# Kernel optimization log

Hardware: AMD Instinct MI355X
Metric: run time of the kernel (lower is better)

## Reference

```python
import jax, jax.numpy as jnp
import numpy as np

N, E, NFEAT, NHID = 50000, 800000, 256, 128
EPS = 1e-5


def setup_inputs() -> dict:
    key = jax.random.key(0)
    ks = jax.random.split(key, 12)
    s = 0.05
    return {
        "x": jax.random.normal(ks[0], (N, NFEAT), jnp.float32),
        "adj": jax.random.randint(ks[1], (2, E), 0, N, jnp.int32),
        "features": jax.random.uniform(ks[2], (E,), jnp.float32),
        "W_in": jax.random.normal(ks[3], (NHID, NFEAT), jnp.float32) * s,
        "b_in": jnp.zeros((NHID,), jnp.float32),
        "W1_rel": jax.random.normal(ks[4], (NHID, NHID), jnp.float32) * s,
        "b1_rel": jnp.zeros((NHID,), jnp.float32),
        "W1_root": jax.random.normal(ks[5], (NHID, NHID), jnp.float32) * s,
        "W2_rel": jax.random.normal(ks[6], (NHID, NHID), jnp.float32) * s,
        "b2_rel": jnp.zeros((NHID,), jnp.float32),
        "W2_root": jax.random.normal(ks[7], (NHID, NHID), jnp.float32) * s,
        "gamma": jnp.ones((NHID,), jnp.float32),
        "beta": jnp.zeros((NHID,), jnp.float32),
    }


def _graph_conv(h, src, dst, ew, W_rel, b_rel, W_root):
    # torch_geometric GraphConv (aggr='add'):
    #   out_i = W_rel @ (sum_{j->i} e_ji * h_j) + b_rel + W_root @ h_i
    msg = h[src] * ew[:, None]                       # [E, NHID] gather
    agg = jax.ops.segment_sum(msg, dst, num_segments=N)  # [N, NHID] scatter-add
    return agg @ W_rel.T + b_rel + h @ W_root.T


def _batch_norm(h, gamma, beta):
    mu = h.mean(axis=0)
    var = h.var(axis=0)
    return (h - mu) * jax.lax.rsqrt(var + EPS) * gamma + beta


def reference(x, adj, features, W_in, b_in, W1_rel, b1_rel, W1_root,
              W2_rel, b2_rel, W2_root, gamma, beta):
    src, dst = adj[0], adj[1]
    h = jax.nn.relu(x @ W_in.T + b_in)               # linear_in + relu (dropout=identity in eval)
    h = _graph_conv(h, src, dst, features, W1_rel, b1_rel, W1_root)
    h = jax.nn.relu(_batch_norm(h, gamma, beta))     # batch1 + relu
    h = _graph_conv(h, src, dst, features, W2_rel, b2_rel, W2_root)
    return _batch_norm(h, gamma, beta)               # batch1 reused (per source)
```

## Files before the change

### kernel.cpp

```cpp
#include <hip/hip_runtime.h>
#include <hip/hip_bf16.h>

#define NNODES 50000
#define NEDGES 800000
#define NF 256
#define NH 128
#define BN_EPS 1e-5f
#define MTILES (NNODES / 16)
#define GEMM_BLOCKS 512
#define CONV_BLOCKS2 512
#define NBUCKETS 196
#define BCAP 4608
#define SCAT_BLOCKS ((NEDGES + 2047) / 2048)
#define WCONV_BLOCKS (98304 / 256)

typedef __attribute__((ext_vector_type(8))) __bf16 bf16x8;
typedef __attribute__((ext_vector_type(4))) float floatx4;

__device__ __forceinline__ __hip_bfloat16 f2bf(float f) { return __float2bfloat16(f); }
__device__ __forceinline__ float bits2f(unsigned short b) {
    union { unsigned u; float f; } u; u.u = ((unsigned)b) << 16; return u.f;
}

__device__ __forceinline__ bf16x8 cvt8(const float* __restrict__ p) {
    floatx4 a0 = *(const floatx4*)p;
    floatx4 a1 = *(const floatx4*)(p + 4);
    bf16x8 r;
    r[0] = (__bf16)a0[0]; r[1] = (__bf16)a0[1]; r[2] = (__bf16)a0[2]; r[3] = (__bf16)a0[3];
    r[4] = (__bf16)a1[0]; r[5] = (__bf16)a1[1]; r[6] = (__bf16)a1[2]; r[7] = (__bf16)a1[3];
    return r;
}

__global__ __launch_bounds__(256) void prep_kernel(
    const int* __restrict__ adj, const float* __restrict__ ew,
    int* __restrict__ gcursor, uint2* __restrict__ pairbuf,
    unsigned char* __restrict__ nodebuf,
    const float* __restrict__ W_in, const float* __restrict__ W1r,
    const float* __restrict__ W1o, const float* __restrict__ W2r,
    const float* __restrict__ W2o, __hip_bfloat16* __restrict__ wbf)
{
    __shared__ int cnt[NBUCKETS];
    __shared__ int base[NBUCKETS];
    const int tid = threadIdx.x;

    if (blockIdx.x >= SCAT_BLOCKS) {
        const int i = (blockIdx.x - SCAT_BLOCKS) * 256 + tid;
        const float* src; int off;
        if (i < 32768)      { src = W_in; off = i; }
        else if (i < 49152) { src = W1r;  off = i - 32768; }
        else if (i < 65536) { src = W1o;  off = i - 49152; }
        else if (i < 81920) { src = W2r;  off = i - 65536; }
        else                { src = W2o;  off = i - 81920; }
        wbf[i] = f2bf(src[off]);
        return;
    }

    if (tid < NBUCKETS) cnt[tid] = 0;
    __syncthreads();
    const int e0 = blockIdx.x * 2048;
    #pragma unroll
    for (int i = 0; i < 8; ++i) {
        const int e = e0 + i * 256 + tid;
        if (e < NEDGES) atomicAdd(&cnt[adj[NEDGES + e] >> 8], 1);
    }
    __syncthreads();
    if (tid < NBUCKETS) {
        base[tid] = tid * BCAP + atomicAdd(&gcursor[tid], cnt[tid]);
        cnt[tid] = 0;
    }
    __syncthreads();
    #pragma unroll
    for (int i = 0; i < 8; ++i) {
        const int e = e0 + i * 256 + tid;
        if (e >= NEDGES) continue;
        const int dst = adj[NEDGES + e];
        const int b = dst >> 8;
        const int off = atomicAdd(&cnt[b], 1);
        const int slot = base[b] + off;
        if (slot < (b + 1) * BCAP) {
            pairbuf[slot] = make_uint2((unsigned)adj[e], __float_as_uint(ew[e]));
            nodebuf[slot] = (unsigned char)(dst & 255);
        }
    }
}

__global__ __launch_bounds__(256) void bucket_sort_kernel(
    const int* __restrict__ gcursor, const uint2* __restrict__ pairbuf,
    const unsigned char* __restrict__ nodebuf, uint2* __restrict__ sorted,
    int* __restrict__ rowptr, int* __restrict__ rowend)
{
    const int b = blockIdx.x;
    const int tid = threadIdx.x;
    const int capbase = b * BCAP;
    int n = gcursor[b];
    if (n > BCAP) n = BCAP;

    __shared__ int cnt[256];
    __shared__ int s[256];
    cnt[tid] = 0;
    __syncthreads();
    for (int j = tid; j < n; j += 256)
        atomicAdd(&cnt[nodebuf[capbase + j]], 1);
    __syncthreads();
    const int v = cnt[tid];
    s[tid] = v;
    __syncthreads();
    for (int off = 1; off < 256; off <<= 1) {
        const int t = (tid >= off) ? s[tid - off] : 0;
        __syncthreads();
        s[tid] += t;
        __syncthreads();
    }
    const int excl = s[tid] - v;
    const int node = b * 256 + tid;
    if (node < NNODES) {
        rowptr[node] = capbase + excl;
        rowend[node] = capbase + excl + v;
    }
    cnt[tid] = excl;
    __syncthreads();
    for (int j = tid; j < n; j += 256) {
        const int nd = nodebuf[capbase + j];
        const int pos = atomicAdd(&cnt[nd], 1);
        sorted[capbase + pos] = pairbuf[capbase + j];
    }
}

__global__ __launch_bounds__(256, 2) void gemm_in_kernel(
    const float* __restrict__ X, const __hip_bfloat16* __restrict__ W,
    const float* __restrict__ bias, __hip_bfloat16* __restrict__ out)
{
    const int waveG = blockIdx.x * 4 + (threadIdx.x >> 6);
    const int lane = threadIdx.x & 63;
    const int half = waveG & 1;
    const int ar = lane & 15;
    const int q  = lane >> 4;

    bf16x8 bw[4][8];
    float bv[4];
    #pragma unroll
    for (int t = 0; t < 4; ++t) {
        const int row = half * 64 + t * 16 + ar;
        bv[t] = bias[row];
        #pragma unroll
        for (int k = 0; k < 8; ++k)
            bw[t][k] = *(const bf16x8*)(W + (size_t)row * NF + k * 32 + q * 8);
    }

    for (int strip = waveG >> 1; strip < MTILES; strip += GEMM_BLOCKS * 2) {
        const int m0 = strip << 4;
        floatx4 acc[4] = {};
        #pragma unroll
        for (int k = 0; k < 8; ++k) {
            const bf16x8 a = cvt8(X + (size_t)(m0 + ar) * NF + k * 32 + q * 8);
            #pragma unroll
            for (int t = 0; t < 4; ++t)
                acc[t] = __builtin_amdgcn_mfma_f32_16x16x32_bf16(a, bw[t][k], acc[t], 0, 0, 0);
        }
        #pragma unroll
        for (int t = 0; t < 4; ++t) {
            const int col = half * 64 + t * 16 + ar;
            #pragma unroll
            for (int r = 0; r < 4; ++r) {
                const float v = fmaxf(acc[t][r] + bv[t], 0.f);
                out[(size_t)(m0 + q * 4 + r) * NH + col] = f2bf(v);
            }
        }
    }
}

__global__ __launch_bounds__(256) void gather_kernel(
    const uint2* __restrict__ sorted, const int* __restrict__ rowptr,
    const int* __restrict__ rowend,
    const __hip_bfloat16* __restrict__ h, __hip_bfloat16* __restrict__ agg)
{
    const int node = blockIdx.x * 4 + (threadIdx.x >> 6);
    if (node >= NNODES) return;
    const int lane = threadIdx.x & 63;
    const int beg = rowptr[node];
    const int end = rowend[node];
    const unsigned short* hb = (const unsigned short*)h;

    float a0[8] = {}, a1[8] = {};

    int j = beg;
    if ((j & 1) && j < end) {
        const uint2 ev = sorted[j++];
        const float w = __uint_as_float(ev.y);
        const unsigned raw = *(const unsigned*)(hb + (size_t)ev.x * NH + lane * 2);
        a0[0] += w * bits2f((unsigned short)(raw & 0xffffu));
        a1[0] += w * bits2f((unsigned short)(raw >> 16));
    }
    for (; j + 8 <= end; j += 8) {
        const uint4 e01 = *(const uint4*)(sorted + j);
        const uint4 e23 = *(const uint4*)(sorted + j + 2);
        const uint4 e45 = *(const uint4*)(sorted + j + 4);
        const uint4 e67 = *(const uint4*)(sorted + j + 6);
        const unsigned r0 = *(const unsigned*)(hb + (size_t)e01.x * NH + lane * 2);
        const unsigned r1 = *(const unsigned*)(hb + (size_t)e01.z * NH + lane * 2);
        const unsigned r2 = *(const unsigned*)(hb + (size_t)e23.x * NH + lane * 2);
        const unsigned r3 = *(const unsigned*)(hb + (size_t)e23.z * NH + lane * 2);
        const unsigned r4 = *(const unsigned*)(hb + (size_t)e45.x * NH + lane * 2);
        const unsigned r5 = *(const unsigned*)(hb + (size_t)e45.z * NH + lane * 2);
        const unsigned r6 = *(const unsigned*)(hb + (size_t)e67.x * NH + lane * 2);
        const unsigned r7 = *(const unsigned*)(hb + (size_t)e67.z * NH + lane * 2);
        const float w0 = __uint_as_float(e01.y), w1 = __uint_as_float(e01.w);
        const float w2 = __uint_as_float(e23.y), w3 = __uint_as_float(e23.w);
        const float w4 = __uint_as_float(e45.y), w5 = __uint_as_float(e45.w);
        const float w6 = __uint_as_float(e67.y), w7 = __uint_as_float(e67.w);
        a0[0] += w0 * bits2f((unsigned short)(r0 & 0xffffu));
        a1[0] += w0 * bits2f((unsigned short)(r0 >> 16));
        a0[1] += w1 * bits2f((unsigned short)(r1 & 0xffffu));
        a1[1] += w1 * bits2f((unsigned short)(r1 >> 16));
        a0[2] += w2 * bits2f((unsigned short)(r2 & 0xffffu));
        a1[2] += w2 * bits2f((unsigned short)(r2 >> 16));
        a0[3] += w3 * bits2f((unsigned short)(r3 & 0xffffu));
        a1[3] += w3 * bits2f((unsigned short)(r3 >> 16));
        a0[4] += w4 * bits2f((unsigned short)(r4 & 0xffffu));
        a1[4] += w4 * bits2f((unsigned short)(r4 >> 16));
        a0[5] += w5 * bits2f((unsigned short)(r5 & 0xffffu));
        a1[5] += w5 * bits2f((unsigned short)(r5 >> 16));
        a0[6] += w6 * bits2f((unsigned short)(r6 & 0xffffu));
        a1[6] += w6 * bits2f((unsigned short)(r6 >> 16));
        a0[7] += w7 * bits2f((unsigned short)(r7 & 0xffffu));
        a1[7] += w7 * bits2f((unsigned short)(r7 >> 16));
    }
    for (; j + 2 <= end; j += 2) {
        const uint4 e01 = *(const uint4*)(sorted + j);
        const unsigned r0 = *(const unsigned*)(hb + (size_t)e01.x * NH + lane * 2);
        const unsigned r1 = *(const unsigned*)(hb + (size_t)e01.z * NH + lane * 2);
        const float w0 = __uint_as_float(e01.y), w1 = __uint_as_float(e01.w);
        a0[0] += w0 * bits2f((unsigned short)(r0 & 0xffffu));
        a1[0] += w0 * bits2f((unsigned short)(r0 >> 16));
        a0[1] += w1 * bits2f((unsigned short)(r1 & 0xffffu));
        a1[1] += w1 * bits2f((unsigned short)(r1 >> 16));
    }
    if (j < end) {
        const uint2 ev = sorted[j];
        const float w = __uint_as_float(ev.y);
        const unsigned raw = *(const unsigned*)(hb + (size_t)ev.x * NH + lane * 2);
        a0[0] += w * bits2f((unsigned short)(raw & 0xffffu));
        a1[0] += w * bits2f((unsigned short)(raw >> 16));
    }
    const float f0 = ((a0[0] + a0[1]) + (a0[2] + a0[3])) + ((a0[4] + a0[5]) + (a0[6] + a0[7]));
    const float f1 = ((a1[0] + a1[1]) + (a1[2] + a1[3])) + ((a1[4] + a1[5]) + (a1[6] + a1[7]));
    unsigned o = ((unsigned)__bfloat16_as_ushort(f2bf(f1)) << 16) |
                 (unsigned)__bfloat16_as_ushort(f2bf(f0));
    *(unsigned*)((unsigned short*)agg + (size_t)node * NH + lane * 2) = o;
}

#define LROW 528

__global__ __launch_bounds__(512, 4) void gemm_conv_kernel(
    const __hip_bfloat16* __restrict__ agg, const __hip_bfloat16* __restrict__ h,
    const __hip_bfloat16* __restrict__ Wrel, const __hip_bfloat16* __restrict__ Wroot,
    const float* __restrict__ bias, float* __restrict__ out,
    float* __restrict__ stats)
{
    __shared__ char wlds[128 * LROW];
    __shared__ float sst[256];
    const int tid = threadIdx.x;
    if (tid < 256) sst[tid] = 0.f;

    {
        const int r = tid >> 2, part = tid & 3;
        const __hip_bfloat16* src = (part < 2 ? Wrel : Wroot) + (size_t)r * NH + (part & 1) * 64;
        char* dst = wlds + r * LROW + part * 128;
        #pragma unroll
        for (int j = 0; j < 8; ++j)
            *(bf16x8*)(dst + j * 16) = *(const bf16x8*)(src + j * 8);
    }
    __syncthreads();

    const int lane = tid & 63;
    const int ar = lane & 15;
    const int q  = lane >> 4;
    const int strip = blockIdx.x * 8 + (tid >> 6);

    if (strip < MTILES) {
        const int m0 = strip << 4;
        float bv[8];
        #pragma unroll
        for (int t = 0; t < 8; ++t) bv[t] = bias[t * 16 + ar];

        floatx4 acc[8] = {};
        const char* wl = wlds + ar * LROW + q * 16;
        #pragma unroll
        for (int kk = 0; kk < 4; ++kk) {
            const bf16x8 a = *(const bf16x8*)(agg + (size_t)(m0 + ar) * NH + kk * 32 + q * 8);
            #pragma unroll
            for (int t = 0; t < 8; ++t)
                acc[t] = __builtin_amdgcn_mfma_f32_16x16x32_bf16(
                    a, *(const bf16x8*)(wl + t * (16 * LROW) + kk * 64), acc[t], 0, 0, 0);
        }
        #pragma unroll
        for (int kk = 0; kk < 4; ++kk) {
            const bf16x8 a = *(const bf16x8*)(h + (size_t)(m0 + ar) * NH + kk * 32 + q * 8);
            #pragma unroll
            for (int t = 0; t < 8; ++t)
                acc[t] = __builtin_amdgcn_mfma_f32_16x16x32_bf16(
                    a, *(const bf16x8*)(wl + t * (16 * LROW) + 256 + kk * 64), acc[t], 0, 0, 0);
        }

        #pragma unroll
        for (int t = 0; t < 8; ++t) {
            float s1 = 0.f, s2 = 0.f;
            #pragma unroll
            for (int r = 0; r < 4; ++r) {
                const float v = acc[t][r] + bv[t];
                out[(size_t)(m0 + q * 4 + r) * NH + t * 16 + ar] = v;
                s1 += v; s2 += v * v;
            }
            s1 += __shfl_xor(s1, 16, 64); s1 += __shfl_xor(s1, 32, 64);
            s2 += __shfl_xor(s2, 16, 64); s2 += __shfl_xor(s2, 32, 64);
            if (q == 0) {
                atomicAdd(&sst[t * 16 + ar], s1);
                atomicAdd(&sst[128 + t * 16 + ar], s2);
            }
        }
    }
    __syncthreads();
    if (tid < 256) unsafeAtomicAdd(&stats[tid], sst[tid]);
}

__global__ __launch_bounds__(256) void bn_relu_bf16_kernel(
    const float* __restrict__ t, const float* __restrict__ stats,
    const float* __restrict__ gamma, const float* __restrict__ beta,
    __hip_bfloat16* __restrict__ out)
{
    const size_t i = (size_t)blockIdx.x * blockDim.x + threadIdx.x;
    const int c = (int)(i & (NH - 1));
    const float inv_n = 1.0f / (float)NNODES;
    const float mu = stats[c] * inv_n;
    const float var = stats[128 + c] * inv_n - mu * mu;
    const float rs = rsqrtf(var + BN_EPS);
    float v = (t[i] - mu) * rs * gamma[c] + beta[c];
    out[i] = f2bf(fmaxf(v, 0.f));
}

__global__ __launch_bounds__(256) void bn_f32_kernel(
    const float* __restrict__ t, const float* __restrict__ stats,
    const float* __restrict__ gamma, const float* __restrict__ beta,
    float* __restrict__ out)
{
    const size_t i = (size_t)blockIdx.x * blockDim.x + threadIdx.x;
    const int c = (int)(i & (NH - 1));
    const float inv_n = 1.0f / (float)NNODES;
    const float mu = stats[c] * inv_n;
    const float var = stats[128 + c] * inv_n - mu * mu;
    const float rs = rsqrtf(var + BN_EPS);
    out[i] = (t[i] - mu) * rs * gamma[c] + beta[c];
}


extern "C" void kernel_launch(void* const* d_in, const int* in_sizes, int n_in,
                              void* d_out, int out_size, void* d_ws, size_t ws_size,
                              hipStream_t stream)
{
    const float* x    = (const float*)d_in[0];
    const int*   adj  = (const int*)d_in[1];
    const float* ew   = (const float*)d_in[2];
    const float* W_in = (const float*)d_in[3];
    const float* b_in = (const float*)d_in[4];
    const float* W1r  = (const float*)d_in[5];
    const float* b1   = (const float*)d_in[6];
    const float* W1o  = (const float*)d_in[7];
    const float* W2r  = (const float*)d_in[8];
    const float* b2   = (const float*)d_in[9];
    const float* W2o  = (const float*)d_in[10];
    const float* gmm  = (const float*)d_in[11];
    const float* bta  = (const float*)d_in[12];
    float* out = (float*)d_out;
    float* t   = (float*)d_out;

    char* ws = (char*)d_ws;
    __hip_bfloat16* h0  = (__hip_bfloat16*)ws; ws += (size_t)NNODES * NH * 2;
    __hip_bfloat16* h1  = (__hip_bfloat16*)ws; ws += (size_t)NNODES * NH * 2;
    __hip_bfloat16* agg = (__hip_bfloat16*)ws; ws += (size_t)NNODES * NH * 2;
    uint2*          sorted  = (uint2*)ws;      ws += (size_t)NBUCKETS * BCAP * 8;
    uint2*          pairbuf = (uint2*)ws;      ws += (size_t)NBUCKETS * BCAP * 8;
    unsigned char*  nodebuf = (unsigned char*)ws; ws += (size_t)NBUCKETS * BCAP;
    int*            rowptr  = (int*)ws;        ws += NNODES * 4;
    int*            rowend  = (int*)ws;        ws += NNODES * 4;
    int*            gcursor = (int*)ws;        ws += 256 * 4;
    float*          st1     = (float*)ws;      ws += 256 * 4;
    float*          st2     = (float*)ws;      ws += 256 * 4;
    __hip_bfloat16* wbf     = (__hip_bfloat16*)ws; ws += 98304 * 2;

    const __hip_bfloat16* Wb_in = wbf;
    const __hip_bfloat16* Wb1r  = wbf + 32768;
    const __hip_bfloat16* Wb1o  = wbf + 49152;
    const __hip_bfloat16* Wb2r  = wbf + 65536;
    const __hip_bfloat16* Wb2o  = wbf + 81920;

    const int node_blocks = (NNODES + 3) / 4;
    const int bn_blocks   = (NNODES * NH) / 256;

    hipMemsetAsync(gcursor, 0, 3 * 256 * 4, stream);
    prep_kernel<<<SCAT_BLOCKS + WCONV_BLOCKS, 256, 0, stream>>>(
        adj, ew, gcursor, pairbuf, nodebuf, W_in, W1r, W1o, W2r, W2o, wbf);
    bucket_sort_kernel<<<NBUCKETS, 256, 0, stream>>>(gcursor, pairbuf, nodebuf,
                                                     sorted, rowptr, rowend);

    gemm_in_kernel<<<GEMM_BLOCKS, 256, 0, stream>>>(x, Wb_in, b_in, h0);
    gather_kernel<<<node_blocks, 256, 0, stream>>>(sorted, rowptr, rowend, h0, agg);
    gemm_conv_kernel<<<CONV_BLOCKS2, 512, 0, stream>>>(agg, h0, Wb1r, Wb1o, b1, t, st1);
    bn_relu_bf16_kernel<<<bn_blocks, 256, 0, stream>>>(t, st1, gmm, bta, h1);

    gather_kernel<<<node_blocks, 256, 0, stream>>>(sorted, rowptr, rowend, h1, agg);
    gemm_conv_kernel<<<CONV_BLOCKS2, 512, 0, stream>>>(agg, h1, Wb2r, Wb2o, b2, t, st2);
    bn_f32_kernel<<<bn_blocks, 256, 0, stream>>>(t, st2, gmm, bta, out);
}
```

Before: 304.9 us.

## Fuse edge gather into graph-conv GEMM via per-wave LDS tile; vectorize BN kernels

Merges the gather kernel and the conv GEMM into one kernel. Each wave aggregates 16 nodes sequentially into an LDS tile, then runs MFMA with weights read directly from global memory instead of staging them in LDS. This removes the agg buffer round trip and one launch per layer. The risk is that gather latency is now serialized per wave, with less parallelism per node and no weight reuse through LDS. The BN kernels are also changed to process four elements per thread with vector loads and stores.

```diff
diff --git a/kernel.cpp b/kernel.cpp
--- a/kernel.cpp
+++ b/kernel.cpp
@@ -8,11 +8,12 @@
 #define BN_EPS 1e-5f
 #define MTILES (NNODES / 16)
 #define GEMM_BLOCKS 512
-#define CONV_BLOCKS2 512
+#define FUSE_BLOCKS ((MTILES + 3) / 4)
 #define NBUCKETS 196
 #define BCAP 4608
 #define SCAT_BLOCKS ((NEDGES + 2047) / 2048)
 #define WCONV_BLOCKS (98304 / 256)
+#define APITCH 272
 
 typedef __attribute__((ext_vector_type(8))) __bf16 bf16x8;
 typedef __attribute__((ext_vector_type(4))) float floatx4;
@@ -169,129 +170,111 @@
     }
 }
 
-__global__ __launch_bounds__(256) void gather_kernel(
+__global__ __launch_bounds__(256, 4) void gather_conv_kernel(
     const uint2* __restrict__ sorted, const int* __restrict__ rowptr,
-    const int* __restrict__ rowend,
-    const __hip_bfloat16* __restrict__ h, __hip_bfloat16* __restrict__ agg)
-{
-    const int node = blockIdx.x * 4 + (threadIdx.x >> 6);
-    if (node >= NNODES) return;
-    const int lane = threadIdx.x & 63;
-    const int beg = rowptr[node];
-    const int end = rowend[node];
-    const unsigned short* hb = (const unsigned short*)h;
-
-    float a0[8] = {}, a1[8] = {};
-
-    int j = beg;
-    if ((j & 1) && j < end) {
-        const uint2 ev = sorted[j++];
-        const float w = __uint_as_float(ev.y);
-        const unsigned raw = *(const unsigned*)(hb + (size_t)ev.x * NH + lane * 2);
-        a0[0] += w * bits2f((unsigned short)(raw & 0xffffu));
-        a1[0] += w * bits2f((unsigned short)(raw >> 16));
-    }
-    for (; j + 8 <= end; j += 8) {
-        const uint4 e01 = *(const uint4*)(sorted + j);
-        const uint4 e23 = *(const uint4*)(sorted + j + 2);
-        const uint4 e45 = *(const uint4*)(sorted + j + 4);
-        const uint4 e67 = *(const uint4*)(sorted + j + 6);
-        const unsigned r0 = *(const unsigned*)(hb + (size_t)e01.x * NH + lane * 2);
-        const unsigned r1 = *(const unsigned*)(hb + (size_t)e01.z * NH + lane * 2);
-        const unsigned r2 = *(const unsigned*)(hb + (size_t)e23.x * NH + lane * 2);
-        const unsigned r3 = *(const unsigned*)(hb + (size_t)e23.z * NH + lane * 2);
-        const unsigned r4 = *(const unsigned*)(hb + (size_t)e45.x * NH + lane * 2);
-        const unsigned r5 = *(const unsigned*)(hb + (size_t)e45.z * NH + lane * 2);
-        const unsigned r6 = *(const unsigned*)(hb + (size_t)e67.x * NH + lane * 2);
-        const unsigned r7 = *(const unsigned*)(hb + (size_t)e67.z * NH + lane * 2);
-        const float w0 = __uint_as_float(e01.y), w1 = __uint_as_float(e01.w);
-        const float w2 = __uint_as_float(e23.y), w3 = __uint_as_float(e23.w);
-        const float w4 = __uint_as_float(e45.y), w5 = __uint_as_float(e45.w);
-        const float w6 = __uint_as_float(e67.y), w7 = __uint_as_float(e67.w);
-        a0[0] += w0 * bits2f((unsigned short)(r0 & 0xffffu));
-        a1[0] += w0 * bits2f((unsigned short)(r0 >> 16));
-        a0[1] += w1 * bits2f((unsigned short)(r1 & 0xffffu));
-        a1[1] += w1 * bits2f((unsigned short)(r1 >> 16));
-        a0[2] += w2 * bits2f((unsigned short)(r2 & 0xffffu));
-        a1[2] += w2 * bits2f((unsigned short)(r2 >> 16));
-        a0[3] += w3 * bits2f((unsigned short)(r3 & 0xffffu));
-        a1[3] += w3 * bits2f((unsigned short)(r3 >> 16));
-        a0[4] += w4 * bits2f((unsigned short)(r4 & 0xffffu));
-        a1[4] += w4 * bits2f((unsigned short)(r4 >> 16));
-        a0[5] += w5 * bits2f((unsigned short)(r5 & 0xffffu));
-        a1[5] += w5 * bits2f((unsigned short)(r5 >> 16));
-        a0[6] += w6 * bits2f((unsigned short)(r6 & 0xffffu));
-        a1[6] += w6 * bits2f((unsigned short)(r6 >> 16));
-        a0[7] += w7 * bits2f((unsigned short)(r7 & 0xffffu));
-        a1[7] += w7 * bits2f((unsigned short)(r7 >> 16));
-    }
-    for (; j + 2 <= end; j += 2) {
-        const uint4 e01 = *(const uint4*)(sorted + j);
-        const unsigned r0 = *(const unsigned*)(hb + (size_t)e01.x * NH + lane * 2);
-        const unsigned r1 = *(const unsigned*)(hb + (size_t)e01.z * NH + lane * 2);
-        const float w0 = __uint_as_float(e01.y), w1 = __uint_as_float(e01.w);
-        a0[0] += w0 * bits2f((unsigned short)(r0 & 0xffffu));
-        a1[0] += w0 * bits2f((unsigned short)(r0 >> 16));
-        a0[1] += w1 * bits2f((unsigned short)(r1 & 0xffffu));
-        a1[1] += w1 * bits2f((unsigned short)(r1 >> 16));
-    }
-    if (j < end) {
-        const uint2 ev = sorted[j];
-        const float w = __uint_as_float(ev.y);
-        const unsigned raw = *(const unsigned*)(hb + (size_t)ev.x * NH + lane * 2);
-        a0[0] += w * bits2f((unsigned short)(raw & 0xffffu));
-        a1[0] += w * bits2f((unsigned short)(raw >> 16));
-    }
-    const float f0 = ((a0[0] + a0[1]) + (a0[2] + a0[3])) + ((a0[4] + a0[5]) + (a0[6] + a0[7]));
-    const float f1 = ((a1[0] + a1[1]) + (a1[2] + a1[3])) + ((a1[4] + a1[5]) + (a1[6] + a1[7]));
-    unsigned o = ((unsigned)__bfloat16_as_ushort(f2bf(f1)) << 16) |
-                 (unsigned)__bfloat16_as_ushort(f2bf(f0));
-    *(unsigned*)((unsigned short*)agg + (size_t)node * NH + lane * 2) = o;
-}
-
-#define LROW 528
-
-__global__ __launch_bounds__(512, 4) void gemm_conv_kernel(
-    const __hip_bfloat16* __restrict__ agg, const __hip_bfloat16* __restrict__ h,
+    const int* __restrict__ rowend, const __hip_bfloat16* __restrict__ h,
     const __hip_bfloat16* __restrict__ Wrel, const __hip_bfloat16* __restrict__ Wroot,
     const float* __restrict__ bias, float* __restrict__ out,
     float* __restrict__ stats)
 {
-    __shared__ char wlds[128 * LROW];
+    __shared__ char alds[4 * 16 * APITCH];
     __shared__ float sst[256];
     const int tid = threadIdx.x;
-    if (tid < 256) sst[tid] = 0.f;
-
-    {
-        const int r = tid >> 2, part = tid & 3;
-        const __hip_bfloat16* src = (part < 2 ? Wrel : Wroot) + (size_t)r * NH + (part & 1) * 64;
-        char* dst = wlds + r * LROW + part * 128;
-        #pragma unroll
-        for (int j = 0; j < 8; ++j)
-            *(bf16x8*)(dst + j * 16) = *(const bf16x8*)(src + j * 8);
-    }
-    __syncthreads();
-
+    sst[tid] = 0.f;
+    __syncthreads();
+
+    const int w = tid >> 6;
     const int lane = tid & 63;
-    const int ar = lane & 15;
-    const int q  = lane >> 4;
-    const int strip = blockIdx.x * 8 + (tid >> 6);
+    const int strip = blockIdx.x * 4 + w;
+    const unsigned short* hb = (const unsigned short*)h;
+    char* atile = alds + w * (16 * APITCH);
 
     if (strip < MTILES) {
         const int m0 = strip << 4;
-        float bv[8];
-        #pragma unroll
-        for (int t = 0; t < 8; ++t) bv[t] = bias[t * 16 + ar];
-
+
+        for (int i = 0; i < 16; ++i) {
+            const int node = m0 + i;
+            const int beg = rowptr[node];
+            const int end = rowend[node];
+
+            float a0[8] = {}, a1[8] = {};
+            int j = beg;
+            if ((j & 1) && j < end) {
+                const uint2 ev = sorted[j++];
+                const float wt = __uint_as_float(ev.y);
+                const unsigned raw = *(const unsigned*)(hb + (size_t)ev.x * NH + lane * 2);
+                a0[0] += wt * bits2f((unsigned short)(raw & 0xffffu));
+                a1[0] += wt * bits2f((unsigned short)(raw >> 16));
+            }
+            for (; j + 8 <= end; j += 8) {
+                const uint4 e01 = *(const uint4*)(sorted + j);
+                const uint4 e23 = *(const uint4*)(sorted + j + 2);
+                const uint4 e45 = *(const uint4*)(sorted + j + 4);
+                const uint4 e67 = *(const uint4*)(sorted + j + 6);
+                const unsigned r0 = *(const unsigned*)(hb + (size_t)e01.x * NH + lane * 2);
+                const unsigned r1 = *(const unsigned*)(hb + (size_t)e01.z * NH + lane * 2);
+                const unsigned r2 = *(const unsigned*)(hb + (size_t)e23.x * NH + lane * 2);
+                const unsigned r3 = *(const unsigned*)(hb + (size_t)e23.z * NH + lane * 2);
+                const unsigned r4 = *(const unsigned*)(hb + (size_t)e45.x * NH + lane * 2);
+                const unsigned r5 = *(const unsigned*)(hb + (size_t)e45.z * NH + lane * 2);
+                const unsigned r6 = *(const unsigned*)(hb + (size_t)e67.x * NH + lane * 2);
+                const unsigned r7 = *(const unsigned*)(hb + (size_t)e67.z * NH + lane * 2);
+                const float w0 = __uint_as_float(e01.y), w1 = __uint_as_float(e01.w);
+                const float w2 = __uint_as_float(e23.y), w3 = __uint_as_float(e23.w);
+                const float w4 = __uint_as_float(e45.y), w5 = __uint_as_float(e45.w);
+                const float w6 = __uint_as_float(e67.y), w7 = __uint_as_float(e67.w);
+                a0[0] += w0 * bits2f((unsigned short)(r0 & 0xffffu));
+                a1[0] += w0 * bits2f((unsigned short)(r0 >> 16));
+                a0[1] += w1 * bits2f((unsigned short)(r1 & 0xffffu));
+                a1[1] += w1 * bits2f((unsigned short)(r1 >> 16));
+                a0[2] += w2 * bits2f((unsigned short)(r2 & 0xffffu));
+                a1[2] += w2 * bits2f((unsigned short)(r2 >> 16));
+                a0[3] += w3 * bits2f((unsigned short)(r3 & 0xffffu));
+                a1[3] += w3 * bits2f((unsigned short)(r3 >> 16));
+                a0[4] += w4 * bits2f((unsigned short)(r4 & 0xffffu));
+                a1[4] += w4 * bits2f((unsigned short)(r4 >> 16));
+                a0[5] += w5 * bits2f((unsigned short)(r5 & 0xffffu));
+                a1[5] += w5 * bits2f((unsigned short)(r5 >> 16));
+                a0[6] += w6 * bits2f((unsigned short)(r6 & 0xffffu));
+                a1[6] += w6 * bits2f((unsigned short)(r6 >> 16));
+                a0[7] += w7 * bits2f((unsigned short)(r7 & 0xffffu));
+                a1[7] += w7 * bits2f((unsigned short)(r7 >> 16));
+            }
+            for (; j + 2 <= end; j += 2) {
+                const uint4 e01 = *(const uint4*)(sorted + j);
+                const unsigned r0 = *(const unsigned*)(hb + (size_t)e01.x * NH + lane * 2);
+                const unsigned r1 = *(const unsigned*)(hb + (size_t)e01.z * NH + lane * 2);
+                const float w0 = __uint_as_float(e01.y), w1 = __uint_as_float(e01.w);
+                a0[0] += w0 * bits2f((unsigned short)(r0 & 0xffffu));
+                a1[0] += w0 * bits2f((unsigned short)(r0 >> 16));
+                a0[1] += w1 * bits2f((unsigned short)(r1 & 0xffffu));
+                a1[1] += w1 * bits2f((unsigned short)(r1 >> 16));
+            }
+            if (j < end) {
+                const uint2 ev = sorted[j];
+                const float wt = __uint_as_float(ev.y);
+                const unsigned raw = *(const unsigned*)(hb + (size_t)ev.x * NH + lane * 2);
+                a0[0] += wt * bits2f((unsigned short)(raw & 0xffffu));
+                a1[0] += wt * bits2f((unsigned short)(raw >> 16));
+            }
+            const float f0 = ((a0[0] + a0[1]) + (a0[2] + a0[3])) + ((a0[4] + a0[5]) + (a0[6] + a0[7]));
+            const float f1 = ((a1[0] + a1[1]) + (a1[2] + a1[3])) + ((a1[4] + a1[5]) + (a1[6] + a1[7]));
+            const unsigned o = ((unsigned)__bfloat16_as_ushort(f2bf(f1)) << 16) |
+                               (unsigned)__bfloat16_as_ushort(f2bf(f0));
+            *(unsigned*)(atile + i * APITCH + lane * 4) = o;
+        }
+
+        const int ar = lane & 15;
+        const int q  = lane >> 4;
         floatx4 acc[8] = {};
-        const char* wl = wlds + ar * LROW + q * 16;
         #pragma unroll
         for (int kk = 0; kk < 4; ++kk) {
-            const bf16x8 a = *(const bf16x8*)(agg + (size_t)(m0 + ar) * NH + kk * 32 + q * 8);
+            const bf16x8 a = *(const bf16x8*)(atile + ar * APITCH + kk * 64 + q * 16);
             #pragma unroll
             for (int t = 0; t < 8; ++t)
                 acc[t] = __builtin_amdgcn_mfma_f32_16x16x32_bf16(
-                    a, *(const bf16x8*)(wl + t * (16 * LROW) + kk * 64), acc[t], 0, 0, 0);
+                    a, *(const bf16x8*)(Wrel + (size_t)(t * 16 + ar) * NH + kk * 32 + q * 8),
+                    acc[t], 0, 0, 0);
         }
         #pragma unroll
         for (int kk = 0; kk < 4; ++kk) {
@@ -299,15 +282,17 @@
             #pragma unroll
             for (int t = 0; t < 8; ++t)
                 acc[t] = __builtin_amdgcn_mfma_f32_16x16x32_bf16(
-                    a, *(const bf16x8*)(wl + t * (16 * LROW) + 256 + kk * 64), acc[t], 0, 0, 0);
+                    a, *(const bf16x8*)(Wroot + (size_t)(t * 16 + ar) * NH + kk * 32 + q * 8),
+                    acc[t], 0, 0, 0);
         }
 
         #pragma unroll
         for (int t = 0; t < 8; ++t) {
+            const float bvt = bias[t * 16 + ar];
             float s1 = 0.f, s2 = 0.f;
             #pragma unroll
             for (int r = 0; r < 4; ++r) {
-                const float v = acc[t][r] + bv[t];
+                const float v = acc[t][r] + bvt;
                 out[(size_t)(m0 + q * 4 + r) * NH + t * 16 + ar] = v;
                 s1 += v; s2 += v * v;
             }
@@ -320,7 +305,7 @@
         }
     }
     __syncthreads();
-    if (tid < 256) unsafeAtomicAdd(&stats[tid], sst[tid]);
+    unsafeAtomicAdd(&stats[tid], sst[tid]);
 }
 
 __global__ __launch_bounds__(256) void bn_relu_bf16_kernel(
@@ -328,14 +313,21 @@
     const float* __restrict__ gamma, const float* __restrict__ beta,
     __hip_bfloat16* __restrict__ out)
 {
-    const size_t i = (size_t)blockIdx.x * blockDim.x + threadIdx.x;
-    const int c = (int)(i & (NH - 1));
+    const size_t i = ((size_t)blockIdx.x * 256 + threadIdx.x) * 4;
     const float inv_n = 1.0f / (float)NNODES;
-    const float mu = stats[c] * inv_n;
-    const float var = stats[128 + c] * inv_n - mu * mu;
-    const float rs = rsqrtf(var + BN_EPS);
-    float v = (t[i] - mu) * rs * gamma[c] + beta[c];
-    out[i] = f2bf(fmaxf(v, 0.f));
+    const floatx4 v = *(const floatx4*)(t + i);
+    ushort4 o;
+    unsigned short* op = (unsigned short*)&o;
+    #pragma unroll
+    for (int j = 0; j < 4; ++j) {
+        const int c = (int)((i + j) & (NH - 1));
+        const float mu = stats[c] * inv_n;
+        const float var = stats[128 + c] * inv_n - mu * mu;
+        const float rs = rsqrtf(var + BN_EPS);
+        const float y = (v[j] - mu) * rs * gamma[c] + beta[c];
+        op[j] = __bfloat16_as_ushort(f2bf(fmaxf(y, 0.f)));
+    }
+    *(ushort4*)((unsigned short*)out + i) = o;
 }
 
 __global__ __launch_bounds__(256) void bn_f32_kernel(
@@ -343,13 +335,19 @@
     const float* __restrict__ gamma, const float* __restrict__ beta,
     float* __restrict__ out)
 {
-    const size_t i = (size_t)blockIdx.x * blockDim.x + threadIdx.x;
-    const int c = (int)(i & (NH - 1));
+    const size_t i = ((size_t)blockIdx.x * 256 + threadIdx.x) * 4;
     const float inv_n = 1.0f / (float)NNODES;
-    const float mu = stats[c] * inv_n;
-    const float var = stats[128 + c] * inv_n - mu * mu;
-    const float rs = rsqrtf(var + BN_EPS);
-    out[i] = (t[i] - mu) * rs * gamma[c] + beta[c];
+    const floatx4 v = *(const floatx4*)(t + i);
+    floatx4 o;
+    #pragma unroll
+    for (int j = 0; j < 4; ++j) {
+        const int c = (int)((i + j) & (NH - 1));
+        const float mu = stats[c] * inv_n;
+        const float var = stats[128 + c] * inv_n - mu * mu;
+        const float rs = rsqrtf(var + BN_EPS);
+        o[j] = (v[j] - mu) * rs * gamma[c] + beta[c];
+    }
+    *(floatx4*)(out + i) = o;
 }
 
 
@@ -376,7 +374,6 @@
     char* ws = (char*)d_ws;
     __hip_bfloat16* h0  = (__hip_bfloat16*)ws; ws += (size_t)NNODES * NH * 2;
     __hip_bfloat16* h1  = (__hip_bfloat16*)ws; ws += (size_t)NNODES * NH * 2;
-    __hip_bfloat16* agg = (__hip_bfloat16*)ws; ws += (size_t)NNODES * NH * 2;
     uint2*          sorted  = (uint2*)ws;      ws += (size_t)NBUCKETS * BCAP * 8;
     uint2*          pairbuf = (uint2*)ws;      ws += (size_t)NBUCKETS * BCAP * 8;
     unsigned char*  nodebuf = (unsigned char*)ws; ws += (size_t)NBUCKETS * BCAP;
@@ -393,8 +390,7 @@
     const __hip_bfloat16* Wb2r  = wbf + 65536;
     const __hip_bfloat16* Wb2o  = wbf + 81920;
 
-    const int node_blocks = (NNODES + 3) / 4;
-    const int bn_blocks   = (NNODES * NH) / 256;
+    const int bn_blocks = (NNODES * NH) / (256 * 4);
 
     hipMemsetAsync(gcursor, 0, 3 * 256 * 4, stream);
     prep_kernel<<<SCAT_BLOCKS + WCONV_BLOCKS, 256, 0, stream>>>(
@@ -403,11 +399,11 @@
                                                      sorted, rowptr, rowend);
 
     gemm_in_kernel<<<GEMM_BLOCKS, 256, 0, stream>>>(x, Wb_in, b_in, h0);
-    gather_kernel<<<node_blocks, 256, 0, stream>>>(sorted, rowptr, rowend, h0, agg);
-    gemm_conv_kernel<<<CONV_BLOCKS2, 512, 0, stream>>>(agg, h0, Wb1r, Wb1o, b1, t, st1);
+    gather_conv_kernel<<<FUSE_BLOCKS, 256, 0, stream>>>(sorted, rowptr, rowend,
+                                                        h0, Wb1r, Wb1o, b1, t, st1);
     bn_relu_bf16_kernel<<<bn_blocks, 256, 0, stream>>>(t, st1, gmm, bta, h1);
 
-    gather_kernel<<<node_blocks, 256, 0, stream>>>(sorted, rowptr, rowend, h1, agg);
-    gemm_conv_kernel<<<CONV_BLOCKS2, 512, 0, stream>>>(agg, h1, Wb2r, Wb2o, b2, t, st2);
+    gather_conv_kernel<<<FUSE_BLOCKS, 256, 0, stream>>>(sorted, rowptr, rowend,
+                                                        h1, Wb2r, Wb2o, b2, t, st2);
     bn_f32_kernel<<<bn_blocks, 256, 0, stream>>>(t, st2, gmm, bta, out);
 }
```

Measured after the change: 372.3 us. 1.22x slower.

## Fuse batchnorm into conv GEMM via grid barrier; merge input GEMM into prep

Applied to the files above, without the earlier changes.

The input linear GEMM moves into the prep kernel as an extra block range, converting W_in to bf16 on the fly, so it runs concurrently with edge bucketing and the weight conversion and saves a launch. The conv GEMM kernels now keep results in registers, accumulate BN statistics, wait at a spin-wait grid barrier on an atomic counter, then apply batchnorm (plus ReLU for layer 1) and write the output directly. This removes the fp32 intermediate write/read and the two separate BN kernels. The risk is that the barrier deadlocks unless all 512 blocks are co-resident, and the spin adds latency.

```diff
diff --git a/kernel.cpp b/kernel.cpp
--- a/kernel.cpp
+++ b/kernel.cpp
@@ -12,7 +12,9 @@
 #define NBUCKETS 196
 #define BCAP 4608
 #define SCAT_BLOCKS ((NEDGES + 2047) / 2048)
-#define WCONV_BLOCKS (98304 / 256)
+#define WC2_BLOCKS 256
+#define FRONT_BLOCKS (SCAT_BLOCKS + WC2_BLOCKS + GEMM_BLOCKS)
+#define LROW 528
 
 typedef __attribute__((ext_vector_type(8))) __bf16 bf16x8;
 typedef __attribute__((ext_vector_type(4))) float floatx4;
@@ -31,33 +33,76 @@
     return r;
 }
 
-__global__ __launch_bounds__(256) void prep_kernel(
+__global__ __launch_bounds__(256, 2) void front_kernel(
     const int* __restrict__ adj, const float* __restrict__ ew,
     int* __restrict__ gcursor, uint2* __restrict__ pairbuf,
     unsigned char* __restrict__ nodebuf,
-    const float* __restrict__ W_in, const float* __restrict__ W1r,
-    const float* __restrict__ W1o, const float* __restrict__ W2r,
-    const float* __restrict__ W2o, __hip_bfloat16* __restrict__ wbf)
+    const float* __restrict__ W1r, const float* __restrict__ W1o,
+    const float* __restrict__ W2r, const float* __restrict__ W2o,
+    __hip_bfloat16* __restrict__ wbf,
+    const float* __restrict__ X, const float* __restrict__ W_in,
+    const float* __restrict__ b_in, __hip_bfloat16* __restrict__ h0)
 {
     __shared__ int cnt[NBUCKETS];
     __shared__ int base[NBUCKETS];
     const int tid = threadIdx.x;
-
-    if (blockIdx.x >= SCAT_BLOCKS) {
-        const int i = (blockIdx.x - SCAT_BLOCKS) * 256 + tid;
+    const int bid = blockIdx.x;
+
+    if (bid >= SCAT_BLOCKS + WC2_BLOCKS) {
+        const int waveG = (bid - SCAT_BLOCKS - WC2_BLOCKS) * 4 + (tid >> 6);
+        const int lane = tid & 63;
+        const int half = waveG & 1;
+        const int ar = lane & 15;
+        const int q  = lane >> 4;
+
+        bf16x8 bw[4][8];
+        float bv[4];
+        #pragma unroll
+        for (int t = 0; t < 4; ++t) {
+            const int row = half * 64 + t * 16 + ar;
+            bv[t] = b_in[row];
+            #pragma unroll
+            for (int k = 0; k < 8; ++k)
+                bw[t][k] = cvt8(W_in + (size_t)row * NF + k * 32 + q * 8);
+        }
+
+        for (int strip = waveG >> 1; strip < MTILES; strip += GEMM_BLOCKS * 2) {
+            const int m0 = strip << 4;
+            floatx4 acc[4] = {};
+            #pragma unroll
+            for (int k = 0; k < 8; ++k) {
+                const bf16x8 a = cvt8(X + (size_t)(m0 + ar) * NF + k * 32 + q * 8);
+                #pragma unroll
+                for (int t = 0; t < 4; ++t)
+                    acc[t] = __builtin_amdgcn_mfma_f32_16x16x32_bf16(a, bw[t][k], acc[t], 0, 0, 0);
+            }
+            #pragma unroll
+            for (int t = 0; t < 4; ++t) {
+                const int col = half * 64 + t * 16 + ar;
+                #pragma unroll
+                for (int r = 0; r < 4; ++r) {
+                    const float v = fmaxf(acc[t][r] + bv[t], 0.f);
+                    h0[(size_t)(m0 + q * 4 + r) * NH + col] = f2bf(v);
+                }
+            }
+        }
+        return;
+    }
+
+    if (bid >= SCAT_BLOCKS) {
+        const int i = (bid - SCAT_BLOCKS) * 256 + tid;
         const float* src; int off;
-        if (i < 32768)      { src = W_in; off = i; }
-        else if (i < 49152) { src = W1r;  off = i - 32768; }
-        else if (i < 65536) { src = W1o;  off = i - 49152; }
-        else if (i < 81920) { src = W2r;  off = i - 65536; }
-        else                { src = W2o;  off = i - 81920; }
+        if (i < 16384)      { src = W1r; off = i; }
+        else if (i < 32768) { src = W1o; off = i - 16384; }
+        else if (i < 49152) { src = W2r; off = i - 32768; }
+        else                { src = W2o; off = i - 49152; }
         wbf[i] = f2bf(src[off]);
         return;
     }
 
     if (tid < NBUCKETS) cnt[tid] = 0;
     __syncthreads();
-    const int e0 = blockIdx.x * 2048;
+    const int e0 = bid * 2048;
     #pragma unroll
     for (int i = 0; i < 8; ++i) {
         const int e = e0 + i * 256 + tid;
@@ -123,49 +168,6 @@
         const int nd = nodebuf[capbase + j];
         const int pos = atomicAdd(&cnt[nd], 1);
         sorted[capbase + pos] = pairbuf[capbase + j];
-    }
-}
-
-__global__ __launch_bounds__(256, 2) void gemm_in_kernel(
-    const float* __restrict__ X, const __hip_bfloat16* __restrict__ W,
-    const float* __restrict__ bias, __hip_bfloat16* __restrict__ out)
-{
-    const int waveG = blockIdx.x * 4 + (threadIdx.x >> 6);
-    const int lane = threadIdx.x & 63;
-    const int half = waveG & 1;
-    const int ar = lane & 15;
-    const int q  = lane >> 4;
-
-    bf16x8 bw[4][8];
-    float bv[4];
-    #pragma unroll
-    for (int t = 0; t < 4; ++t) {
-        const int row = half * 64 + t * 16 + ar;
-        bv[t] = bias[row];
-        #pragma unroll
-        for (int k = 0; k < 8; ++k)
-            bw[t][k] = *(const bf16x8*)(W + (size_t)row * NF + k * 32 + q * 8);
-    }
-
-    for (int strip = waveG >> 1; strip < MTILES; strip += GEMM_BLOCKS * 2) {
-        const int m0 = strip << 4;
-        floatx4 acc[4] = {};
-        #pragma unroll
-        for (int k = 0; k < 8; ++k) {
-            const bf16x8 a = cvt8(X + (size_t)(m0 + ar) * NF + k * 32 + q * 8);
-            #pragma unroll
-            for (int t = 0; t < 4; ++t)
-                acc[t] = __builtin_amdgcn_mfma_f32_16x16x32_bf16(a, bw[t][k], acc[t], 0, 0, 0);
-        }
-        #pragma unroll
-        for (int t = 0; t < 4; ++t) {
-            const int col = half * 64 + t * 16 + ar;
-            #pragma unroll
-            for (int r = 0; r < 4; ++r) {
-                const float v = fmaxf(acc[t][r] + bv[t], 0.f);
-                out[(size_t)(m0 + q * 4 + r) * NH + col] = f2bf(v);
-            }
-        }
     }
 }
 
@@ -249,13 +251,13 @@
     *(unsigned*)((unsigned short*)agg + (size_t)node * NH + lane * 2) = o;
 }
 
-#define LROW 528
-
-__global__ __launch_bounds__(512, 4) void gemm_conv_kernel(
+template<int LAYER>
+__global__ __launch_bounds__(512, 4) void conv_bn_kernel(
     const __hip_bfloat16* __restrict__ agg, const __hip_bfloat16* __restrict__ h,
     const __hip_bfloat16* __restrict__ Wrel, const __hip_bfloat16* __restrict__ Wroot,
-    const float* __restrict__ bias, float* __restrict__ out,
-    float* __restrict__ stats)
+    const float* __restrict__ bias, const float* __restrict__ gamma,
+    const float* __restrict__ beta, float* __restrict__ stats,
+    int* __restrict__ ctr, void* __restrict__ outv)
 {
     __shared__ char wlds[128 * LROW];
     __shared__ float sst[256];
@@ -276,14 +278,15 @@
     const int ar = lane & 15;
     const int q  = lane >> 4;
     const int strip = blockIdx.x * 8 + (tid >> 6);
+    const int m0 = strip << 4;
+
+    floatx4 acc[8] = {};
+    float bv[8];
 
     if (strip < MTILES) {
-        const int m0 = strip << 4;
-        float bv[8];
         #pragma unroll
         for (int t = 0; t < 8; ++t) bv[t] = bias[t * 16 + ar];
 
-        floatx4 acc[8] = {};
         const char* wl = wlds + ar * LROW + q * 16;
         #pragma unroll
         for (int kk = 0; kk < 4; ++kk) {
@@ -308,7 +311,6 @@
             #pragma unroll
             for (int r = 0; r < 4; ++r) {
                 const float v = acc[t][r] + bv[t];
-                out[(size_t)(m0 + q * 4 + r) * NH + t * 16 + ar] = v;
                 s1 += v; s2 += v * v;
             }
             s1 += __shfl_xor(s1, 16, 64); s1 += __shfl_xor(s1, 32, 64);
@@ -321,35 +323,43 @@
     }
     __syncthreads();
     if (tid < 256) unsafeAtomicAdd(&stats[tid], sst[tid]);
-}
-
-__global__ __launch_bounds__(256) void bn_relu_bf16_kernel(
-    const float* __restrict__ t, const float* __restrict__ stats,
-    const float* __restrict__ gamma, const float* __restrict__ beta,
-    __hip_bfloat16* __restrict__ out)
-{
-    const size_t i = (size_t)blockIdx.x * blockDim.x + threadIdx.x;
-    const int c = (int)(i & (NH - 1));
-    const float inv_n = 1.0f / (float)NNODES;
-    const float mu = stats[c] * inv_n;
-    const float var = stats[128 + c] * inv_n - mu * mu;
-    const float rs = rsqrtf(var + BN_EPS);
-    float v = (t[i] - mu) * rs * gamma[c] + beta[c];
-    out[i] = f2bf(fmaxf(v, 0.f));
-}
-
-__global__ __launch_bounds__(256) void bn_f32_kernel(
-    const float* __restrict__ t, const float* __restrict__ stats,
-    const float* __restrict__ gamma, const float* __restrict__ beta,
-    float* __restrict__ out)
-{
-    const size_t i = (size_t)blockIdx.x * blockDim.x + threadIdx.x;
-    const int c = (int)(i & (NH - 1));
-    const float inv_n = 1.0f / (float)NNODES;
-    const float mu = stats[c] * inv_n;
-    const float var = stats[128 + c] * inv_n - mu * mu;
-    const float rs = rsqrtf(var + BN_EPS);
-    out[i] = (t[i] - mu) * rs * gamma[c] + beta[c];
+    __syncthreads();
+
+    if (tid == 0) {
+        __threadfence();
+        __hip_atomic_fetch_add(ctr, 1, __ATOMIC_ACQ_REL, __HIP_MEMORY_SCOPE_AGENT);
+        while (__hip_atomic_load(ctr, __ATOMIC_ACQUIRE, __HIP_MEMORY_SCOPE_AGENT)
+               < CONV_BLOCKS2)
+            __builtin_amdgcn_s_sleep(8);
+    }
+    __syncthreads();
+
+    if (tid < 256)
+        sst[tid] = __hip_atomic_load(&stats[tid], __ATOMIC_RELAXED, __HIP_MEMORY_SCOPE_AGENT);
+    __syncthreads();
+
+    if (strip < MTILES) {
+        const float inv_n = 1.0f / (float)NNODES;
+        #pragma unroll
+        for (int t = 0; t < 8; ++t) {
+            const int col = t * 16 + ar;
+            const float mu = sst[col] * inv_n;
+            const float var = sst[128 + col] * inv_n - mu * mu;
+            const float rsg = rsqrtf(var + BN_EPS) * gamma[col];
+            const float bt = beta[col];
+            #pragma unroll
+            for (int r = 0; r < 4; ++r) {
+                const float v = acc[t][r] + bv[t];
+                const float y = (v - mu) * rsg + bt;
+                if (LAYER == 0) {
+                    ((__hip_bfloat16*)outv)[(size_t)(m0 + q * 4 + r) * NH + col] =
+                        f2bf(fmaxf(y, 0.f));
+                } else {
+                    ((float*)outv)[(size_t)(m0 + q * 4 + r) * NH + col] = y;
+                }
+            }
+        }
+    }
 }
 
 
@@ -371,7 +381,6 @@
     const float* gmm  = (const float*)d_in[11];
     const float* bta  = (const float*)d_in[12];
     float* out = (float*)d_out;
-    float* t   = (float*)d_out;
 
     char* ws = (char*)d_ws;
     __hip_bfloat16* h0  = (__hip_bfloat16*)ws; ws += (size_t)NNODES * NH * 2;
@@ -385,29 +394,28 @@
     int*            gcursor = (int*)ws;        ws += 256 * 4;
     float*          st1     = (float*)ws;      ws += 256 * 4;
     float*          st2     = (float*)ws;      ws += 256 * 4;
-    __hip_bfloat16* wbf     = (__hip_bfloat16*)ws; ws += 98304 * 2;
-
-    const __hip_bfloat16* Wb_in = wbf;
-    const __hip_bfloat16* Wb1r  = wbf + 32768;
-    const __hip_bfloat16* Wb1o  = wbf + 49152;
-    const __hip_bfloat16* Wb2r  = wbf + 65536;
-    const __hip_bfloat16* Wb2o  = wbf + 81920;
+    int*            ctr     = (int*)ws;        ws += 256 * 4;
+    __hip_bfloat16* wbf     = (__hip_bfloat16*)ws; ws += 65536 * 2;
+
+    const __hip_bfloat16* Wb1r = wbf;
+    const __hip_bfloat16* Wb1o = wbf + 16384;
+    const __hip_bfloat16* Wb2r = wbf + 32768;
+    const __hip_bfloat16* Wb2o = wbf + 49152;
 
     const int node_blocks = (NNODES + 3) / 4;
-    const int bn_blocks   = (NNODES * NH) / 256;
-
-    hipMemsetAsync(gcursor, 0, 3 * 256 * 4, stream);
-    prep_kernel<<<SCAT_BLOCKS + WCONV_BLOCKS, 256, 0, stream>>>(
-        adj, ew, gcursor, pairbuf, nodebuf, W_in, W1r, W1o, W2r, W2o, wbf);
+
+    hipMemsetAsync(gcursor, 0, 4 * 256 * 4, stream);
+    front_kernel<<<FRONT_BLOCKS, 256, 0, stream>>>(
+        adj, ew, gcursor, pairbuf, nodebuf, W1r, W1o, W2r, W2o, wbf,
+        x, W_in, b_in, h0);
     bucket_sort_kernel<<<NBUCKETS, 256, 0, stream>>>(gcursor, pairbuf, nodebuf,
                                                      sorted, rowptr, rowend);
 
-    gemm_in_kernel<<<GEMM_BLOCKS, 256, 0, stream>>>(x, Wb_in, b_in, h0);
     gather_kernel<<<node_blocks, 256, 0, stream>>>(sorted, rowptr, rowend, h0, agg);
-    gemm_conv_kernel<<<CONV_BLOCKS2, 512, 0, stream>>>(agg, h0, Wb1r, Wb1o, b1, t, st1);
-    bn_relu_bf16_kernel<<<bn_blocks, 256, 0, stream>>>(t, st1, gmm, bta, h1);
+    conv_bn_kernel<0><<<CONV_BLOCKS2, 512, 0, stream>>>(agg, h0, Wb1r, Wb1o, b1,
+                                                        gmm, bta, st1, ctr, (void*)h1);
 
     gather_kernel<<<node_blocks, 256, 0, stream>>>(sorted, rowptr, rowend, h1, agg);
-    gemm_conv_kernel<<<CONV_BLOCKS2, 512, 0, stream>>>(agg, h1, Wb2r, Wb2o, b2, t, st2);
-    bn_f32_kernel<<<bn_blocks, 256, 0, stream>>>(t, st2, gmm, bta, out);
-}
+    conv_bn_kernel<1><<<CONV_BLOCKS2, 512, 0, stream>>>(agg, h1, Wb2r, Wb2o, b2,
+                                                        gmm, bta, st2, ctr + 1, (void*)out);
+}
```

Result: slower. 365.6 us (+19.9%).
